# Kernel tuning notes

Hardware: AMD Instinct MI355X
Metric: run time of the kernel (lower is better)

Reference implementation:

```python
import jax, jax.numpy as jnp
import numpy as np

N = 50000          # nodes
E = 400000         # random edges (self-loops added in reference, per PyG default)
IN, HID, HEADS, OUT = 20, 64, 4, 256
NEG_SLOPE = 0.2    # GATv2Conv default negative_slope
EPS = 1e-16        # PyG softmax denom epsilon


def setup_inputs() -> dict:
    key = jax.random.key(0)
    ks = jax.random.split(key, 14)
    g = lambda k, shape, scale=0.1: (jax.random.normal(k, shape, jnp.float32) * scale)
    return {
        "x": jax.random.normal(ks[0], (N, IN), jnp.float32),
        "edge_index": jax.random.randint(ks[1], (2, E), 0, N, jnp.int32),
        # layer 1: GATv2Conv(IN -> HID, heads=HEADS, concat=True)
        "W_l1": g(ks[2], (IN, HEADS * HID)),
        "b_l1": jnp.zeros((HEADS * HID,), jnp.float32),
        "W_r1": g(ks[3], (IN, HEADS * HID)),
        "b_r1": jnp.zeros((HEADS * HID,), jnp.float32),
        "att1": g(ks[4], (HEADS, HID)),
        "bias1": jnp.zeros((HEADS * HID,), jnp.float32),
        # layer 2: GATv2Conv(HEADS*HID -> OUT, heads=1, concat=False)
        "W_l2": g(ks[5], (HEADS * HID, OUT)),
        "b_l2": jnp.zeros((OUT,), jnp.float32),
        "W_r2": g(ks[6], (HEADS * HID, OUT)),
        "b_r2": jnp.zeros((OUT,), jnp.float32),
        "att2": g(ks[7], (1, OUT)),
        "bias2": jnp.zeros((OUT,), jnp.float32),
    }


def _gatv2_layer(x, src, dst, W_l, b_l, W_r, b_r, att, bias, heads, ch, concat):
    n = x.shape[0]
    x_l = (x @ W_l + b_l).reshape(n, heads, ch)  # source transform
    x_r = (x @ W_r + b_r).reshape(n, heads, ch)  # target transform
    # GATv2: e_ij = att . LeakyReLU(x_l[j] + x_r[i])   (j->i edge)
    pre = jax.nn.leaky_relu(x_l[src] + x_r[dst], NEG_SLOPE)       # [E, H, C]
    logits = jnp.einsum('ehc,hc->eh', pre, att)                    # [E, H]
    # segment softmax over destination node (self-loops guarantee nonempty)
    m = jax.ops.segment_max(logits, dst, num_segments=n)
    w = jnp.exp(logits - m[dst])
    denom = jax.ops.segment_sum(w, dst, num_segments=n)
    alpha = w / (denom[dst] + EPS)                                 # [E, H]
    out = jax.ops.segment_sum(x_l[src] * alpha[:, :, None], dst, num_segments=n)
    out = out.reshape(n, heads * ch) if concat else out.mean(axis=1)
    return out + bias


def reference(x, edge_index, W_l1, b_l1, W_r1, b_r1, att1, bias1,
              W_l2, b_l2, W_r2, b_r2, att2, bias2):
    n = x.shape[0]
    loop = jnp.arange(n, dtype=edge_index.dtype)  # PyG add_self_loops=True
    src = jnp.concatenate([edge_index[0], loop])
    dst = jnp.concatenate([edge_index[1], loop])
    h = _gatv2_layer(x, src, dst, W_l1, b_l1, W_r1, b_r1, att1, bias1, HEADS, HID, True)
    h = jax.nn.elu(h)
    out = _gatv2_layer(h, src, dst, W_l2, b_l2, W_r2, b_r2, att2, bias2, 1, OUT, False)
    return out
```

## Files before the change

kernel.cpp:

```cpp
#include <hip/hip_runtime.h>
#include <hip/hip_bf16.h>
#include <math.h>

#define CH 256
#define SCAN_BLOCK 1024

typedef short bf16x8 __attribute__((ext_vector_type(8)));
typedef float f32x4 __attribute__((ext_vector_type(4)));

__device__ __forceinline__ float lrelu(float v) { return fmaxf(v, 0.2f * v); }
__device__ __forceinline__ float elu(float v)   { return v > 0.f ? v : __expf(v) - 1.f; }

__device__ __forceinline__ unsigned short f2bf(float f) {
    unsigned u = __float_as_uint(f);
    return (unsigned short)((u + 0x7fffu + ((u >> 16) & 1u)) >> 16);
}
__device__ __forceinline__ float4 ldbf4(const unsigned short* rowbase, int lane) {
    uint2 u = ((const uint2*)rowbase)[lane];
    return make_float4(__uint_as_float(u.x << 16), __uint_as_float(u.x & 0xffff0000u),
                       __uint_as_float(u.y << 16), __uint_as_float(u.y & 0xffff0000u));
}
__device__ __forceinline__ void stbf4(unsigned short* rowbase, int lane, float4 v) {
    uint2 u;
    u.x = (unsigned)f2bf(v.x) | ((unsigned)f2bf(v.y) << 16);
    u.y = (unsigned)f2bf(v.z) | ((unsigned)f2bf(v.w) << 16);
    ((uint2*)rowbase)[lane] = u;
}

__global__ __launch_bounds__(256) void gemm1_kernel(const float* __restrict__ x,
                             const float* __restrict__ Wl, const float* __restrict__ bl,
                             const float* __restrict__ Wr, const float* __restrict__ br,
                             unsigned short* __restrict__ xl, unsigned short* __restrict__ xr, int n) {
    __shared__ float xs[64][20];
    int n0 = blockIdx.x * 64;
    int tid = threadIdx.x;
    for (int i = tid; i < 64 * 20; i += 256) {
        int m = i / 20, k = i % 20;
        int row = n0 + m;
        xs[m][k] = (row < n) ? x[(size_t)row * 20 + k] : 0.f;
    }
    int c = tid;
    float wl[20], wr[20];
#pragma unroll
    for (int k = 0; k < 20; ++k) { wl[k] = Wl[k * 256 + c]; wr[k] = Wr[k * 256 + c]; }
    float blv = bl[c], brv = br[c];
    __syncthreads();
#pragma unroll 1
    for (int g = 0; g < 8; ++g) {
        int base = g * 8;
        float al[8], ar[8];
#pragma unroll
        for (int m = 0; m < 8; ++m) { al[m] = blv; ar[m] = brv; }
#pragma unroll
        for (int k = 0; k < 20; ++k) {
            float wlv = wl[k], wrv = wr[k];
#pragma unroll
            for (int m = 0; m < 8; ++m) {
                float xv = xs[base + m][k];
                al[m] += xv * wlv;
                ar[m] += xv * wrv;
            }
        }
#pragma unroll
        for (int m = 0; m < 8; ++m) {
            int row = n0 + base + m;
            if (row < n) {
                xl[(size_t)row * 256 + c] = f2bf(al[m]);
                xr[(size_t)row * 256 + c] = f2bf(ar[m]);
            }
        }
    }
}

__global__ void count_deg(const int* __restrict__ ei, int* __restrict__ deg, int e) {
    int t = blockIdx.x * blockDim.x + threadIdx.x;
    if (t < e) atomicAdd(&deg[ei[e + t]], 1);
}

__global__ void scan_block_k(const int* __restrict__ deg, int* __restrict__ rowptr,
                             int* __restrict__ bsums, int n) {
    __shared__ int wsum[16];
    __shared__ int woff[17];
    int tid = threadIdx.x;
    int gi = blockIdx.x * SCAN_BLOCK + tid;
    int lane = tid & 63, wid = tid >> 6;
    int v = (gi < n) ? deg[gi] : 0;
    int incl = v;
#pragma unroll
    for (int d = 1; d < 64; d <<= 1) {
        int t = __shfl_up(incl, d, 64);
        if (lane >= d) incl += t;
    }
    if (lane == 63) wsum[wid] = incl;
    __syncthreads();
    if (tid < 16) {
        int s = wsum[tid];
#pragma unroll
        for (int d = 1; d < 16; d <<= 1) {
            int t = __shfl_up(s, d, 64);
            if (tid >= d) s += t;
        }
        woff[tid + 1] = s;
        if (tid == 0) woff[0] = 0;
    }
    __syncthreads();
    incl += woff[wid];
    if (gi < n) rowptr[gi + 1] = incl;
    if (tid == 0) bsums[blockIdx.x] = woff[16];
}

__global__ void scan_tops_k(int* bsums, int nb) {
    int tid = threadIdx.x;
    int v = (tid < nb) ? bsums[tid] : 0;
    int incl = v;
#pragma unroll
    for (int d = 1; d < 64; d <<= 1) {
        int t = __shfl_up(incl, d, 64);
        if (tid >= d) incl += t;
    }
    if (tid < nb) bsums[tid] = incl - v;
}

__global__ void scan_fix_k(int* __restrict__ rowptr, int* __restrict__ cursor,
                           const int* __restrict__ deg, const int* __restrict__ bsums, int n) {
    int gi = blockIdx.x * SCAN_BLOCK + threadIdx.x;
    if (gi >= n) return;
    int off = bsums[blockIdx.x];
    int incl = rowptr[gi + 1] + off;
    rowptr[gi + 1] = incl;
    cursor[gi] = incl - deg[gi];
    if (gi == 0) rowptr[0] = 0;
}

__global__ void scatter_k(const int* __restrict__ ei, int* __restrict__ cursor,
                          int* __restrict__ csr, int e) {
    int t = blockIdx.x * blockDim.x + threadIdx.x;
    if (t >= e) return;
    int s = ei[t], d = ei[e + t];
    int idx = atomicAdd(&cursor[d], 1);
    csr[idx] = s;
}

__global__ void fused_gat1(const unsigned short* __restrict__ xl, const unsigned short* __restrict__ xr,
                           const int* __restrict__ rowptr, const int* __restrict__ csr,
                           const float* __restrict__ att, const float* __restrict__ bias,
                           unsigned short* __restrict__ hout, int n) {
    int wid = threadIdx.x >> 6;
    int lane = threadIdx.x & 63;
    int i = blockIdx.x * 4 + wid;
    if (i >= n) return;
    float4 xr4 = ldbf4(xr + (size_t)i * CH, lane);
    float4 a4  = ((const float4*)att)[lane];
    float4 xli = ldbf4(xl + (size_t)i * CH, lane);
    float ps = lrelu(xli.x + xr4.x) * a4.x + lrelu(xli.y + xr4.y) * a4.y +
               lrelu(xli.z + xr4.z) * a4.z + lrelu(xli.w + xr4.w) * a4.w;
    ps += __shfl_xor(ps, 1); ps += __shfl_xor(ps, 2);
    ps += __shfl_xor(ps, 4); ps += __shfl_xor(ps, 8);
    float m = ps, l = 1.f;
    float4 acc = xli;
    int beg = rowptr[i], end = rowptr[i + 1];
    for (int e = beg; e < end; e += 4) {
        int cnt = end - e;
        int s0 = csr[e];
        int s1 = (cnt > 1) ? csr[e + 1] : s0;
        int s2 = (cnt > 2) ? csr[e + 2] : s0;
        int s3 = (cnt > 3) ? csr[e + 3] : s0;
        float4 r0 = ldbf4(xl + (size_t)s0 * CH, lane);
        float4 r1 = ldbf4(xl + (size_t)s1 * CH, lane);
        float4 r2 = ldbf4(xl + (size_t)s2 * CH, lane);
        float4 r3 = ldbf4(xl + (size_t)s3 * CH, lane);
        float p0 = lrelu(r0.x + xr4.x) * a4.x + lrelu(r0.y + xr4.y) * a4.y +
                   lrelu(r0.z + xr4.z) * a4.z + lrelu(r0.w + xr4.w) * a4.w;
        float p1 = lrelu(r1.x + xr4.x) * a4.x + lrelu(r1.y + xr4.y) * a4.y +
                   lrelu(r1.z + xr4.z) * a4.z + lrelu(r1.w + xr4.w) * a4.w;
        float p2 = lrelu(r2.x + xr4.x) * a4.x + lrelu(r2.y + xr4.y) * a4.y +
                   lrelu(r2.z + xr4.z) * a4.z + lrelu(r2.w + xr4.w) * a4.w;
        float p3 = lrelu(r3.x + xr4.x) * a4.x + lrelu(r3.y + xr4.y) * a4.y +
                   lrelu(r3.z + xr4.z) * a4.z + lrelu(r3.w + xr4.w) * a4.w;
        p0 += __shfl_xor(p0, 1); p1 += __shfl_xor(p1, 1); p2 += __shfl_xor(p2, 1); p3 += __shfl_xor(p3, 1);
        p0 += __shfl_xor(p0, 2); p1 += __shfl_xor(p1, 2); p2 += __shfl_xor(p2, 2); p3 += __shfl_xor(p3, 2);
        p0 += __shfl_xor(p0, 4); p1 += __shfl_xor(p1, 4); p2 += __shfl_xor(p2, 4); p3 += __shfl_xor(p3, 4);
        p0 += __shfl_xor(p0, 8); p1 += __shfl_xor(p1, 8); p2 += __shfl_xor(p2, 8); p3 += __shfl_xor(p3, 8);
        if (cnt < 2) p1 = -INFINITY;
        if (cnt < 3) p2 = -INFINITY;
        if (cnt < 4) p3 = -INFINITY;
        float mn = fmaxf(m, fmaxf(fmaxf(p0, p1), fmaxf(p2, p3)));
        float sc = __expf(m - mn);
        float w0 = __expf(p0 - mn), w1 = __expf(p1 - mn);
        float w2 = __expf(p2 - mn), w3 = __expf(p3 - mn);
        l = l * sc + w0 + w1 + w2 + w3;
        acc.x = acc.x * sc + w0 * r0.x + w1 * r1.x + w2 * r2.x + w3 * r3.x;
        acc.y = acc.y * sc + w0 * r0.y + w1 * r1.y + w2 * r2.y + w3 * r3.y;
        acc.z = acc.z * sc + w0 * r0.z + w1 * r1.z + w2 * r2.z + w3 * r3.z;
        acc.w = acc.w * sc + w0 * r0.w + w1 * r1.w + w2 * r2.w + w3 * r3.w;
        m = mn;
    }
    float inv = 1.f / (l + 1e-16f);
    float4 b4 = ((const float4*)bias)[lane];
    float4 o;
    o.x = elu(acc.x * inv + b4.x);
    o.y = elu(acc.y * inv + b4.y);
    o.z = elu(acc.z * inv + b4.z);
    o.w = elu(acc.w * inv + b4.w);
    stbf4(hout + (size_t)i * CH, lane, o);
}

__global__ void fused_gat2(const unsigned short* __restrict__ xl, const unsigned short* __restrict__ xr,
                           const int* __restrict__ rowptr, const int* __restrict__ csr,
                           const float* __restrict__ att, const float* __restrict__ bias,
                           float* __restrict__ out, int n) {
    int wid = threadIdx.x >> 6;
    int lane = threadIdx.x & 63;
    int i = blockIdx.x * 4 + wid;
    if (i >= n) return;
    float4 xr4 = ldbf4(xr + (size_t)i * CH, lane);
    float4 a4  = ((const float4*)att)[lane];
    float4 xli = ldbf4(xl + (size_t)i * CH, lane);
    float ps = lrelu(xli.x + xr4.x) * a4.x + lrelu(xli.y + xr4.y) * a4.y +
               lrelu(xli.z + xr4.z) * a4.z + lrelu(xli.w + xr4.w) * a4.w;
    ps += __shfl_xor(ps, 1); ps += __shfl_xor(ps, 2); ps += __shfl_xor(ps, 4);
    ps += __shfl_xor(ps, 8); ps += __shfl_xor(ps, 16); ps += __shfl_xor(ps, 32);
    float m = ps, l = 1.f;
    float4 acc = xli;
    int beg = rowptr[i], end = rowptr[i + 1];
    for (int e = beg; e < end; e += 4) {
        int cnt = end - e;
        int s0 = csr[e];
        int s1 = (cnt > 1) ? csr[e + 1] : s0;
        int s2 = (cnt > 2) ? csr[e + 2] : s0;
        int s3 = (cnt > 3) ? csr[e + 3] : s0;
        float4 r0 = ldbf4(xl + (size_t)s0 * CH, lane);
        float4 r1 = ldbf4(xl + (size_t)s1 * CH, lane);
        float4 r2 = ldbf4(xl + (size_t)s2 * CH, lane);
        float4 r3 = ldbf4(xl + (size_t)s3 * CH, lane);
        float p0 = lrelu(r0.x + xr4.x) * a4.x + lrelu(r0.y + xr4.y) * a4.y +
                   lrelu(r0.z + xr4.z) * a4.z + lrelu(r0.w + xr4.w) * a4.w;
        float p1 = lrelu(r1.x + xr4.x) * a4.x + lrelu(r1.y + xr4.y) * a4.y +
                   lrelu(r1.z + xr4.z) * a4.z + lrelu(r1.w + xr4.w) * a4.w;
        float p2 = lrelu(r2.x + xr4.x) * a4.x + lrelu(r2.y + xr4.y) * a4.y +
                   lrelu(r2.z + xr4.z) * a4.z + lrelu(r2.w + xr4.w) * a4.w;
        float p3 = lrelu(r3.x + xr4.x) * a4.x + lrelu(r3.y + xr4.y) * a4.y +
                   lrelu(r3.z + xr4.z) * a4.z + lrelu(r3.w + xr4.w) * a4.w;
#pragma unroll
        for (int d = 1; d < 64; d <<= 1) {
            p0 += __shfl_xor(p0, d); p1 += __shfl_xor(p1, d);
            p2 += __shfl_xor(p2, d); p3 += __shfl_xor(p3, d);
        }
        if (cnt < 2) p1 = -INFINITY;
        if (cnt < 3) p2 = -INFINITY;
        if (cnt < 4) p3 = -INFINITY;
        float mn = fmaxf(m, fmaxf(fmaxf(p0, p1), fmaxf(p2, p3)));
        float sc = __expf(m - mn);
        float w0 = __expf(p0 - mn), w1 = __expf(p1 - mn);
        float w2 = __expf(p2 - mn), w3 = __expf(p3 - mn);
        l = l * sc + w0 + w1 + w2 + w3;
        acc.x = acc.x * sc + w0 * r0.x + w1 * r1.x + w2 * r2.x + w3 * r3.x;
        acc.y = acc.y * sc + w0 * r0.y + w1 * r1.y + w2 * r2.y + w3 * r3.y;
        acc.z = acc.z * sc + w0 * r0.z + w1 * r1.z + w2 * r2.z + w3 * r3.z;
        acc.w = acc.w * sc + w0 * r0.w + w1 * r1.w + w2 * r2.w + w3 * r3.w;
        m = mn;
    }
    float inv = 1.f / (l + 1e-16f);
    float4 b4 = ((const float4*)bias)[lane];
    float4 o;
    o.x = acc.x * inv + b4.x;
    o.y = acc.y * inv + b4.y;
    o.z = acc.z * inv + b4.z;
    o.w = acc.w * inv + b4.w;
    ((float4*)(out + (size_t)i * CH))[lane] = o;
}

__global__ void wconv(const float* __restrict__ Wl2, const float* __restrict__ Wr2,
                      unsigned short* __restrict__ Wt) {
    int t = blockIdx.x * 256 + threadIdx.x;
    int z = t >> 16;
    int idx = t & 65535;
    int k = idx >> 8, nn = idx & 255;
    const float* W = z ? Wr2 : Wl2;
    Wt[z * 65536 + nn * 256 + k] = f2bf(W[k * 256 + nn]);
}

#define LDK 40
__global__ __launch_bounds__(256) void gemm_mfma(
        const unsigned short* __restrict__ A,
        const unsigned short* __restrict__ Wt,
        const float* __restrict__ ba, const float* __restrict__ bb,
        unsigned short* __restrict__ Ca, unsigned short* __restrict__ Cb, int M) {
    const unsigned short* Wz = Wt + (size_t)blockIdx.z * 65536;
    const float* bias = blockIdx.z ? bb : ba;
    unsigned short* C = blockIdx.z ? Cb : Ca;

    __shared__ unsigned short As[128 * LDK];
    __shared__ unsigned short Bs[128 * LDK];

    int m0 = blockIdx.x * 128, n0 = blockIdx.y * 128;
    int tid = threadIdx.x;
    int lane = tid & 63, wid = tid >> 6;
    int wm = wid & 1, wn = wid >> 1;
    int q = lane >> 4, l15 = lane & 15;

    f32x4 acc[4][4];
#pragma unroll
    for (int i = 0; i < 4; ++i)
#pragma unroll
        for (int j = 0; j < 4; ++j) acc[i][j] = (f32x4){0.f, 0.f, 0.f, 0.f};

    int r = tid >> 2;
    int c8 = (tid & 3) * 8;
    const uint4 zero4 = make_uint4(0, 0, 0, 0);

    for (int kb = 0; kb < 8; ++kb) {
        int k0 = kb * 32;
        int ra = m0 + r, rb = m0 + r + 64;
        uint4 va0 = (ra < M) ? *(const uint4*)(A + (size_t)ra * 256 + k0 + c8) : zero4;
        uint4 va1 = (rb < M) ? *(const uint4*)(A + (size_t)rb * 256 + k0 + c8) : zero4;
        uint4 vb0 = *(const uint4*)(Wz + (size_t)(n0 + r) * 256 + k0 + c8);
        uint4 vb1 = *(const uint4*)(Wz + (size_t)(n0 + r + 64) * 256 + k0 + c8);
        __syncthreads();
        *(uint4*)&As[r * LDK + c8] = va0;
        *(uint4*)&As[(r + 64) * LDK + c8] = va1;
        *(uint4*)&Bs[r * LDK + c8] = vb0;
        *(uint4*)&Bs[(r + 64) * LDK + c8] = vb1;
        __syncthreads();

        bf16x8 af[4], bfr[4];
#pragma unroll
        for (int f = 0; f < 4; ++f)
            af[f] = *(const bf16x8*)&As[(wm * 64 + f * 16 + l15) * LDK + q * 8];
#pragma unroll
        for (int f = 0; f < 4; ++f)
            bfr[f] = *(const bf16x8*)&Bs[(wn * 64 + f * 16 + l15) * LDK + q * 8];
#pragma unroll
        for (int i = 0; i < 4; ++i)
#pragma unroll
            for (int j = 0; j < 4; ++j)
                acc[i][j] = __builtin_amdgcn_mfma_f32_16x16x32_bf16(af[i], bfr[j], acc[i][j], 0, 0, 0);
    }

#pragma unroll
    for (int j = 0; j < 4; ++j) {
        int gcol = n0 + wn * 64 + j * 16 + l15;
        float bcol = bias[gcol];
#pragma unroll
        for (int i = 0; i < 4; ++i) {
            int row = m0 + wm * 64 + i * 16 + q * 4;
#pragma unroll
            for (int rr = 0; rr < 4; ++rr) {
                int grow = row + rr;
                if (grow < M)
                    C[(size_t)grow * 256 + gcol] = f2bf(acc[i][j][rr] + bcol);
            }
        }
    }
}

extern "C" void kernel_launch(void* const* d_in, const int* in_sizes, int n_in,
                              void* d_out, int out_size, void* d_ws, size_t ws_size,
                              hipStream_t stream) {
    const float* x    = (const float*)d_in[0];
    const int*   ei   = (const int*)d_in[1];
    const float* Wl1  = (const float*)d_in[2];
    const float* bl1  = (const float*)d_in[3];
    const float* Wr1  = (const float*)d_in[4];
    const float* br1  = (const float*)d_in[5];
    const float* att1 = (const float*)d_in[6];
    const float* bias1= (const float*)d_in[7];
    const float* Wl2  = (const float*)d_in[8];
    const float* bl2  = (const float*)d_in[9];
    const float* Wr2  = (const float*)d_in[10];
    const float* br2  = (const float*)d_in[11];
    const float* att2 = (const float*)d_in[12];
    const float* bias2= (const float*)d_in[13];

    int n = in_sizes[0] / 20;
    int e = in_sizes[1] / 2;
    float* out = (float*)d_out;
    size_t nch = (size_t)n * CH;

    unsigned short* buf0 = (unsigned short*)d_ws;
    unsigned short* buf1 = buf0 + nch;
    unsigned short* hbuf = buf1 + nch;
    unsigned short* wt2  = hbuf + nch;
    int* deg    = (int*)(wt2 + 2 * 65536);
    int* rowptr = deg + n;
    int* cursor = rowptr + n + 1;
    int* bsums  = cursor + n;
    int* csr    = bsums + 64;

    hipMemsetAsync(deg, 0, (size_t)n * sizeof(int), stream);

    gemm1_kernel<<<(n + 63) / 64, 256, 0, stream>>>(x, Wl1, bl1, Wr1, br1, buf0, buf1, n);

    count_deg<<<(e + 255) / 256, 256, 0, stream>>>(ei, deg, e);
    int nb = (n + SCAN_BLOCK - 1) / SCAN_BLOCK;
    scan_block_k<<<nb, SCAN_BLOCK, 0, stream>>>(deg, rowptr, bsums, n);
    scan_tops_k<<<1, 64, 0, stream>>>(bsums, nb);
    scan_fix_k<<<nb, SCAN_BLOCK, 0, stream>>>(rowptr, cursor, deg, bsums, n);
    scatter_k<<<(e + 255) / 256, 256, 0, stream>>>(ei, cursor, csr, e);

    wconv<<<512, 256, 0, stream>>>(Wl2, Wr2, wt2);

    fused_gat1<<<(n + 3) / 4, 256, 0, stream>>>(buf0, buf1, rowptr, csr, att1, bias1, hbuf, n);

    gemm_mfma<<<dim3((n + 127) / 128, 2, 2), 256, 0, stream>>>(hbuf, wt2, bl2, br2, buf0, buf1, n);

    fused_gat2<<<(n + 3) / 4, 256, 0, stream>>>(buf0, buf1, rowptr, csr, att2, bias2, out, n);
}
```

Before: 321.4 us.

## Double-buffer MFMA GEMM tiles with direct global-to-LDS loads

The layer-2 bf16 GEMM now stages A and W tiles straight into LDS with global_load_lds, using two buffers so the next k-slice loads while MFMAs run on the current one. The padded LDS stride is dropped for an unpadded 32-element layout, as the direct-to-LDS load writes contiguous rows. Out-of-range A rows are clamped to the last row instead of being zero-filled; those results are never stored. The intent is to hide global load latency and remove the register round trip and one barrier per k step, at the risk of LDS bank conflicts on fragment reads and an unclear wait on the async loads before the barrier.

```diff
diff --git a/kernel.cpp b/kernel.cpp
--- a/kernel.cpp
+++ b/kernel.cpp
@@ -25,6 +25,12 @@
     u.x = (unsigned)f2bf(v.x) | ((unsigned)f2bf(v.y) << 16);
     u.y = (unsigned)f2bf(v.z) | ((unsigned)f2bf(v.w) << 16);
     ((uint2*)rowbase)[lane] = u;
+}
+
+typedef const __attribute__((address_space(1))) unsigned int* gas_p;
+typedef __attribute__((address_space(3))) unsigned int* las_p;
+__device__ __forceinline__ void gload16(const unsigned short* g, unsigned short* l) {
+    __builtin_amdgcn_global_load_lds((gas_p)g, (las_p)l, 16, 0, 0);
 }
 
 __global__ __launch_bounds__(256) void gemm1_kernel(const float* __restrict__ x,
@@ -280,7 +286,7 @@
     Wt[z * 65536 + nn * 256 + k] = f2bf(W[k * 256 + nn]);
 }
 
-#define LDK 40
+#define LDE 32
 __global__ __launch_bounds__(256) void gemm_mfma(
         const unsigned short* __restrict__ A,
         const unsigned short* __restrict__ Wt,
@@ -290,8 +296,8 @@
     const float* bias = blockIdx.z ? bb : ba;
     unsigned short* C = blockIdx.z ? Cb : Ca;
 
-    __shared__ unsigned short As[128 * LDK];
-    __shared__ unsigned short Bs[128 * LDK];
+    __shared__ unsigned short As[2][128 * LDE];
+    __shared__ unsigned short Bs[2][128 * LDE];
 
     int m0 = blockIdx.x * 128, n0 = blockIdx.y * 128;
     int tid = threadIdx.x;
@@ -299,43 +305,59 @@
     int wm = wid & 1, wn = wid >> 1;
     int q = lane >> 4, l15 = lane & 15;
 
+    int lr = lane >> 2;
+    int lc = (lane & 3) * 8;
+    int Mm1 = M - 1;
+    int ra0 = m0 + wid * 32 + lr;      if (ra0 > Mm1) ra0 = Mm1;
+    int ra1 = m0 + wid * 32 + 16 + lr; if (ra1 > Mm1) ra1 = Mm1;
+    const unsigned short* pa0 = A  + (size_t)ra0 * 256 + lc;
+    const unsigned short* pa1 = A  + (size_t)ra1 * 256 + lc;
+    const unsigned short* pb0 = Wz + (size_t)(n0 + wid * 32 + lr) * 256 + lc;
+    const unsigned short* pb1 = Wz + (size_t)(n0 + wid * 32 + 16 + lr) * 256 + lc;
+    unsigned short* da0; unsigned short* da1; unsigned short* db0; unsigned short* db1;
+
     f32x4 acc[4][4];
 #pragma unroll
     for (int i = 0; i < 4; ++i)
 #pragma unroll
         for (int j = 0; j < 4; ++j) acc[i][j] = (f32x4){0.f, 0.f, 0.f, 0.f};
 
-    int r = tid >> 2;
-    int c8 = (tid & 3) * 8;
-    const uint4 zero4 = make_uint4(0, 0, 0, 0);
-
+#define STAGE(b, kb) do {                                   \
+        int koff = (kb) * 32;                               \
+        da0 = &As[b][(wid * 32) * LDE];                     \
+        da1 = &As[b][(wid * 32 + 16) * LDE];                \
+        db0 = &Bs[b][(wid * 32) * LDE];                     \
+        db1 = &Bs[b][(wid * 32 + 16) * LDE];                \
+        gload16(pa0 + koff, da0);                           \
+        gload16(pa1 + koff, da1);                           \
+        gload16(pb0 + koff, db0);                           \
+        gload16(pb1 + koff, db1);                           \
+    } while (0)
+
+    STAGE(0, 0);
+    __syncthreads();
+
+#pragma unroll
     for (int kb = 0; kb < 8; ++kb) {
-        int k0 = kb * 32;
-        int ra = m0 + r, rb = m0 + r + 64;
-        uint4 va0 = (ra < M) ? *(const uint4*)(A + (size_t)ra * 256 + k0 + c8) : zero4;
-        uint4 va1 = (rb < M) ? *(const uint4*)(A + (size_t)rb * 256 + k0 + c8) : zero4;
-        uint4 vb0 = *(const uint4*)(Wz + (size_t)(n0 + r) * 256 + k0 + c8);
-        uint4 vb1 = *(const uint4*)(Wz + (size_t)(n0 + r + 64) * 256 + k0 + c8);
-        __syncthreads();
-        *(uint4*)&As[r * LDK + c8] = va0;
-        *(uint4*)&As[(r + 64) * LDK + c8] = va1;
-        *(uint4*)&Bs[r * LDK + c8] = vb0;
-        *(uint4*)&Bs[(r + 64) * LDK + c8] = vb1;
-        __syncthreads();
+        int cur = kb & 1;
+        if (kb < 7) STAGE(cur ^ 1, kb + 1);
 
         bf16x8 af[4], bfr[4];
 #pragma unroll
         for (int f = 0; f < 4; ++f)
-            af[f] = *(const bf16x8*)&As[(wm * 64 + f * 16 + l15) * LDK + q * 8];
+            af[f] = *(const bf16x8*)&As[cur][(wm * 64 + f * 16 + l15) * LDE + q * 8];
 #pragma unroll
         for (int f = 0; f < 4; ++f)
-            bfr[f] = *(const bf16x8*)&Bs[(wn * 64 + f * 16 + l15) * LDK + q * 8];
+            bfr[f] = *(const bf16x8*)&Bs[cur][(wn * 64 + f * 16 + l15) * LDE + q * 8];
 #pragma unroll
         for (int i = 0; i < 4; ++i)
 #pragma unroll
             for (int j = 0; j < 4; ++j)
                 acc[i][j] = __builtin_amdgcn_mfma_f32_16x16x32_bf16(af[i], bfr[j], acc[i][j], 0, 0, 0);
-    }
+
+        __syncthreads();
+    }
+#undef STAGE
 
 #pragma unroll
     for (int j = 0; j < 4; ++j) {
```

New measurement: 319.5 us. Within noise of the previous version (-0.6%).
